# Performance work log

Measured on AMD Instinct MI355X. Metric: run time of the kernel, lower is better.

The kernel has to match this reference:

```python
import jax, jax.numpy as jnp
import numpy as np

EMBED_DIM = 512
NUM_HEADS = 8
GLOBAL_MIX = 0.5


def setup_inputs() -> dict:
    key = jax.random.key(0)
    ks = jax.random.split(key, 7)
    B, L, E = 8, 1024, EMBED_DIM
    s = 1.0 / np.sqrt(E)
    x = jax.random.normal(ks[0], (B, L, E), dtype=jnp.float32)
    mask = jax.random.randint(ks[1], (B, L), 0, 2) > 0  # True = valid token
    Wq = jax.random.normal(ks[2], (E, E), dtype=jnp.float32) * s
    Wk = jax.random.normal(ks[3], (E, E), dtype=jnp.float32) * s
    Wv = jax.random.normal(ks[4], (E, E), dtype=jnp.float32) * s
    Wo = jax.random.normal(ks[5], (E, E), dtype=jnp.float32) * s
    G = jax.random.normal(ks[6], (L, L), dtype=jnp.float32)
    return {"x": x, "mask": mask, "Wq": Wq, "Wk": Wk, "Wv": Wv, "Wo": Wo, "G": G}


def _tanh_mha(x, mask, Wq, Wk, Wv, Wo, G):
    B, L, E = x.shape
    H = NUM_HEADS
    D = E // H
    scale = 1.0 / np.sqrt(D)
    dt = x.dtype
    fmax = jnp.finfo(dt).max
    tiny = jnp.finfo(dt).tiny

    def split_heads(t):  # (B,L,E) -> (B,H,L,D)
        return t.reshape(B, L, H, D).transpose(0, 2, 1, 3)

    q = split_heads(x @ Wq.T)
    k = split_heads(x @ Wk.T)
    v = split_heads(x @ Wv.T)

    scores = jnp.tanh(jnp.einsum('bhqd,bhkd->bhqk', q, k) * scale)
    key_valid = mask[:, None, None, :]  # (B,1,1,L)
    scores = jnp.where(key_valid, scores, -jnp.inf)

    finite = jnp.isfinite(scores)
    finite_scores = jnp.where(finite, scores, -fmax)
    m = jnp.max(finite_scores, axis=(1, 2, 3), keepdims=True)  # per-sample amax over heads+q+k
    m = jnp.where(jnp.isfinite(m), m, jnp.zeros_like(m))
    exp_scores = jnp.where(finite, jnp.exp(scores - m), jnp.zeros_like(scores))

    mf = mask.astype(dt)
    exp_scores = exp_scores * mf[:, None, None, :] * mf[:, None, :, None]
    denom = jnp.maximum(exp_scores.sum(axis=(1, 2, 3), keepdims=True), tiny)
    weights = exp_scores / denom
    # dropout p=0 -> identity; renorm pass kept for faithfulness
    renorm = jnp.maximum(weights.sum(axis=(1, 2, 3), keepdims=True), tiny)
    weights = weights / renorm

    # learnable global attention: softmax rows, clamp, mask, normalize over (q,k)
    activated = jnp.maximum(jax.nn.softmax(G, axis=-1), 0.0)  # (L,L)
    gscores = activated[None] * mf[:, None, :] * mf[:, :, None]  # (B,L,L)
    gsums = jnp.maximum(gscores.sum(axis=(1, 2), keepdims=True), tiny)
    gnorm = (gscores / gsums)[:, None]  # (B,1,L,L)
    weights = (1.0 - GLOBAL_MIX) * weights + GLOBAL_MIX * gnorm

    attended = jnp.einsum('bhqk,bhkd->bhqd', weights, v)
    attended = attended * mf[:, None, :, None]
    attended = attended.transpose(0, 2, 1, 3).reshape(B, L, E)
    return attended @ Wo.T


def reference(x, mask, Wq, Wk, Wv, Wo, G):
    return _tanh_mha(x, mask, Wq, Wk, Wv, Wo, G)
```

## Files before the change

kernel.cpp:

```cpp
#include <hip/hip_runtime.h>
#include <math.h>

#define B_ 8
#define L_ 1024
#define E_ 512
#define H_ 8
#define D_ 64
#define QSZ (B_*H_*L_*D_)
#define BLE ((size_t)B_*L_*E_)
#define TINYF 1.175494350822287508e-38f
#define SWK(r) ((((r) ^ ((r) >> 3))) & 7)

typedef unsigned short u16;
typedef __attribute__((ext_vector_type(8))) short bfrag;
typedef __attribute__((ext_vector_type(4))) float ffrag;
typedef __attribute__((ext_vector_type(16))) float ffrag16;
typedef __attribute__((ext_vector_type(4))) short vshort4;

#if __has_builtin(__builtin_amdgcn_exp2f)
#define EXP2F(x) __builtin_amdgcn_exp2f(x)
#else
#define EXP2F(x) __expf((x) * 0.6931471805599453f)
#endif
#if __has_builtin(__builtin_amdgcn_rcpf)
#define RCPF(x) __builtin_amdgcn_rcpf(x)
#else
#define RCPF(x) (1.0f / (x))
#endif

__device__ __forceinline__ u16 f2b(float f) {
  unsigned u = __float_as_uint(f);
  u += 0x7fffu + ((u >> 16) & 1u);
  return (u16)(u >> 16);
}
__device__ __forceinline__ unsigned pk2(float a, float b) {
  unsigned ua = __float_as_uint(a); ua += 0x7fffu + ((ua >> 16) & 1u);
  unsigned ub = __float_as_uint(b); ub += 0x7fffu + ((ub >> 16) & 1u);
  return (ua >> 16) | (ub & 0xffff0000u);
}
__device__ __forceinline__ float blo(unsigned u) { return __uint_as_float(u << 16); }
__device__ __forceinline__ float bhi(unsigned u) { return __uint_as_float(u & 0xffff0000u); }

__device__ __forceinline__ bfrag cvt8v(const float* __restrict__ src) {
  float4 a = *(const float4*)src;
  float4 b = *(const float4*)(src + 4);
  bfrag r;
  r[0]=(short)f2b(a.x); r[1]=(short)f2b(a.y); r[2]=(short)f2b(a.z); r[3]=(short)f2b(a.w);
  r[4]=(short)f2b(b.x); r[5]=(short)f2b(b.y); r[6]=(short)f2b(b.z); r[7]=(short)f2b(b.w);
  return r;
}

__device__ __forceinline__ void gll16(const void* g, void* l) {
  __builtin_amdgcn_global_load_lds(
      (const __attribute__((address_space(1))) void*)g,
      (__attribute__((address_space(3))) void*)l, 16, 0, 0);
}

__global__ __launch_bounds__(256) void prep_softmax_k(
    const float* __restrict__ x, const float* __restrict__ Wq,
    const float* __restrict__ Wk, const float* __restrict__ Wv,
    const float* __restrict__ Wo, const float* __restrict__ G,
    const int* __restrict__ mask,
    u16* __restrict__ xb, u16* __restrict__ Wb, u16* __restrict__ actb,
    float* __restrict__ R) {
  const int bid = blockIdx.x, t = threadIdx.x;
  __shared__ float sred[8];
  __shared__ float rred[4][8];
  if (bid < 2048) {
    size_t c = (size_t)bid * 256 + t;
    *(bfrag*)&xb[c * 8] = cvt8v(x + c * 8);
    return;
  }
  if (bid < 2560) {
    const int c2 = bid - 2048;
    const float* src = (c2 < 128) ? Wq : (c2 < 256) ? Wk : (c2 < 384) ? Wv : Wo;
    const size_t base = (size_t)(c2 >> 7) * 262144;
    const size_t cc = (size_t)(c2 & 127) * 256 + t;
    *(bfrag*)&Wb[base + cc * 8] = cvt8v(src + cc * 8);
    return;
  }
  const int q = bid - 2560;
  const int w = t >> 6, lane = t & 63;
  float4 g4 = ((const float4*)(G + (size_t)q * 1024))[t];
  float m = fmaxf(fmaxf(g4.x, g4.y), fmaxf(g4.z, g4.w));
#pragma unroll
  for (int off = 32; off > 0; off >>= 1) m = fmaxf(m, __shfl_down(m, off));
  if (lane == 0) sred[w] = m;
  __syncthreads();
  m = fmaxf(fmaxf(sred[0], sred[1]), fmaxf(sred[2], sred[3]));
  float e0 = __expf(g4.x - m), e1 = __expf(g4.y - m);
  float e2 = __expf(g4.z - m), e3 = __expf(g4.w - m);
  float s = e0 + e1 + e2 + e3;
#pragma unroll
  for (int off = 32; off > 0; off >>= 1) s += __shfl_down(s, off);
  if (lane == 0) sred[4 + w] = s;
  __syncthreads();
  const float inv = 1.0f / (sred[4] + sred[5] + sred[6] + sred[7]);
  const unsigned p0 = pk2(e0 * inv, e1 * inv);
  const unsigned p1 = pk2(e2 * inv, e3 * inv);
  *(uint2*)&actb[(size_t)q * 1024 + t * 4] = make_uint2(p0, p1);
  const float r0 = blo(p0), r1 = bhi(p0);
  const float r2 = blo(p1), r3 = bhi(p1);
  float rd[8];
#pragma unroll
  for (int b = 0; b < 8; ++b) {
    const int* mkp = mask + b * 1024 + t * 4;
    rd[b] = (mkp[0] ? r0 : 0.f) + (mkp[1] ? r1 : 0.f) +
            (mkp[2] ? r2 : 0.f) + (mkp[3] ? r3 : 0.f);
#pragma unroll
    for (int off = 32; off > 0; off >>= 1) rd[b] += __shfl_down(rd[b], off);
  }
  if (lane == 0)
#pragma unroll
    for (int b = 0; b < 8; ++b) rred[w][b] = rd[b];
  __syncthreads();
  if (t < 8) R[q * 8 + t] = rred[0][t] + rred[1][t] + rred[2][t] + rred[3][t];
}

__global__ __launch_bounds__(256) void proj_k(
    const u16* __restrict__ xb, const u16* __restrict__ Wb,
    const int* __restrict__ mask, const float* __restrict__ R,
    float* __restrict__ sums,
    u16* __restrict__ Qb, u16* __restrict__ Kb, u16* __restrict__ Vtb) {
  const int m0 = blockIdx.x * 128;
  const int n0 = blockIdx.y * 128;
  __shared__ __align__(16) u16 As[128 * 64];
  __shared__ __align__(16) u16 Bs[128 * 64];
  __shared__ float rr[4][8];
  const int t = threadIdx.x, w = t >> 6, lane = t & 63;
  const int l15 = lane & 15, quad = lane >> 4;
  const int mq = (w >> 1) * 64, nq = (w & 1) * 64;

  if (blockIdx.x == 0 && blockIdx.y == 0) {
    float a8[8] = {0,0,0,0,0,0,0,0};
    for (int q = t; q < 1024; q += 256)
#pragma unroll
      for (int b = 0; b < 8; ++b)
        if (mask[b * 1024 + q]) a8[b] += R[q * 8 + b];
#pragma unroll
    for (int b = 0; b < 8; ++b) {
#pragma unroll
      for (int off = 32; off > 0; off >>= 1) a8[b] += __shfl_down(a8[b], off);
    }
    if (lane == 0)
#pragma unroll
      for (int b = 0; b < 8; ++b) rr[w][b] = a8[b];
    __syncthreads();
    if (t < 8) {
      sums[t] = 0.0f;
      sums[8 + t] = rr[0][t] + rr[1][t] + rr[2][t] + rr[3][t];
    }
  }

  const ffrag fz = {0.f, 0.f, 0.f, 0.f};
  ffrag acc[4][4];
#pragma unroll
  for (int i = 0; i < 4; ++i)
#pragma unroll
    for (int j = 0; j < 4; ++j) acc[i][j] = fz;

  for (int kk = 0; kk < 512; kk += 64) {
    __syncthreads();
#pragma unroll
    for (int j = 0; j < 4; ++j) {
      const int c = w * 256 + j * 64 + lane;
      const int row = c >> 3, ck = (c & 7) ^ (row & 7);
      gll16(xb + (size_t)(m0 + row) * 512 + kk + ck * 8,
            &As[(size_t)(w * 256 + j * 64) * 8]);
    }
#pragma unroll
    for (int j = 0; j < 4; ++j) {
      const int c = w * 256 + j * 64 + lane;
      const int row = c >> 3, ck = (c & 7) ^ (row & 7);
      gll16(Wb + (size_t)(n0 + row) * 512 + kk + ck * 8,
            &Bs[(size_t)(w * 256 + j * 64) * 8]);
    }
    __syncthreads();
#pragma unroll
    for (int s = 0; s < 2; ++s) {
      bfrag av[4], bv[4];
#pragma unroll
      for (int i = 0; i < 4; ++i) {
        const int ar = mq + i * 16 + l15;
        av[i] = *(const bfrag*)&As[ar * 64 + (((quad + 4 * s) ^ (ar & 7)) << 3)];
        const int br = nq + i * 16 + l15;
        bv[i] = *(const bfrag*)&Bs[br * 64 + (((quad + 4 * s) ^ (br & 7)) << 3)];
      }
#pragma unroll
      for (int i = 0; i < 4; ++i)
#pragma unroll
        for (int j = 0; j < 4; ++j)
          acc[i][j] = __builtin_amdgcn_mfma_f32_16x16x32_bf16(av[i], bv[j], acc[i][j], 0, 0, 0);
    }
  }
  const int z = n0 >> 9;
  const int c0 = n0 & 511;
#pragma unroll
  for (int i = 0; i < 4; ++i) {
    const int mbase = m0 + mq + i * 16 + quad * 4;
    const int b = mbase >> 10, l0 = mbase & 1023;
#pragma unroll
    for (int j = 0; j < 4; ++j) {
      const int nc = c0 + nq + j * 16 + l15;
      const int h = nc >> 6, d = nc & 63;
      if (z == 0) {
        u16* dst = Qb + ((size_t)(b * 8 + h) * 1024 + l0) * 64 + d;
#pragma unroll
        for (int r = 0; r < 4; ++r) dst[(size_t)r * 64] = f2b(acc[i][j][r]);
      } else if (z == 1) {
        u16* dst = Kb + ((size_t)(b * 8 + h) * 1024 + l0) * 64 + d;
#pragma unroll
        for (int r = 0; r < 4; ++r) dst[(size_t)r * 64] = f2b(acc[i][j][r]);
      } else {
        vshort4 vs;
#pragma unroll
        for (int r = 0; r < 4; ++r)
          vs[r] = (short)(mask[b * 1024 + l0 + r] ? f2b(acc[i][j][r]) : (u16)0);
        *(vshort4*)(Vtb + ((size_t)(b * 8 + h) * 64 + d) * 1024 + l0) = vs;
      }
    }
  }
}

__global__ __launch_bounds__(256) void attn_k(
    const u16* __restrict__ Qb, const u16* __restrict__ Kb,
    const u16* __restrict__ Vtb, const u16* __restrict__ actb,
    const int* __restrict__ mask,
    u16* __restrict__ AEb, u16* __restrict__ AGb, float* __restrict__ denom) {
  const int qt = blockIdx.x;
  const int bh = blockIdx.y;
  const int b = bh >> 3, h = bh & 7;
  __shared__ __align__(16) u16 Ks[64 * 64];
  __shared__ __align__(16) u16 Vs[64 * 64];
  __shared__ __align__(16) u16 Acts[64 * 64];
  __shared__ __align__(16) u16 Es[64 * 64];
  __shared__ __align__(16) u16 Ms[1024];
  __shared__ float red4[4];
  const int t = threadIdx.x, w = t >> 6, lane = t & 63;
  const int l31 = lane & 31, hi = lane >> 5;
  const int qsb = w >> 1, msb = w & 1;
  const int qpb = w & 1, dpb = w >> 1;

  const u16* Kg = Kb + (size_t)bh * 65536;
  const u16* Vg = Vtb + (size_t)bh * 65536;
  const u16* Ag = actb + (size_t)(qt * 64) * 1024;

  const u16* Qrow = Qb + ((size_t)bh * 1024 + qt * 64 + qsb * 32 + l31) * 64;
  bfrag qf[4];
#pragma unroll
  for (int ko = 0; ko < 4; ++ko) qf[ko] = *(const bfrag*)(Qrow + ko * 16 + hi * 8);

  {
    int4 mi = *(const int4*)(mask + b * 1024 + t * 4);
    vshort4 mv;
    mv[0] = mi.x ? (short)0x3F80 : (short)0; mv[1] = mi.y ? (short)0x3F80 : (short)0;
    mv[2] = mi.z ? (short)0x3F80 : (short)0; mv[3] = mi.w ? (short)0x3F80 : (short)0;
    *(vshort4*)&Ms[t * 4] = mv;
  }

  auto stageK = [&](int kt) {
#pragma unroll
    for (int j = 0; j < 2; ++j) {
      const int c = w * 128 + j * 64 + lane;
      const int row = c >> 3, ck = (c & 7) ^ SWK(row);
      gll16(Kg + (size_t)(kt * 64 + row) * 64 + ck * 8,
            &Ks[(size_t)(w * 128 + j * 64) * 8]);
    }
  };
  auto stageV = [&](int kt) {
#pragma unroll
    for (int j = 0; j < 2; ++j) {
      const int c = w * 128 + j * 64 + lane;
      const int row = c >> 3, ck = (c & 7) ^ SWK(row);
      gll16(Vg + (size_t)row * 1024 + kt * 64 + ck * 8,
            &Vs[(size_t)(w * 128 + j * 64) * 8]);
    }
  };
  auto stageA = [&](int kt) {
#pragma unroll
    for (int j = 0; j < 2; ++j) {
      const int c = w * 128 + j * 64 + lane;
      const int row = c >> 3, ck = (c & 7) ^ SWK(row);
      gll16(Ag + (size_t)row * 1024 + kt * 64 + ck * 8,
            &Acts[(size_t)(w * 128 + j * 64) * 8]);
    }
  };

  stageK(0); stageV(0); stageA(0);
  __syncthreads();

  ffrag16 accE, accG, dacc;
#pragma unroll
  for (int i = 0; i < 16; ++i) { accE[i] = 0.f; accG[i] = 0.f; dacc[i] = 0.f; }

  for (int kt = 0; kt < 16; ++kt) {
    ffrag16 st;
#pragma unroll
    for (int i = 0; i < 16; ++i) st[i] = 0.f;
    const int krow = msb * 32 + l31;
    const int kk7 = SWK(krow);
#pragma unroll
    for (int ko = 0; ko < 4; ++ko) {
      bfrag ak = *(const bfrag*)&Ks[krow * 64 + (((ko * 2 + hi) ^ kk7) << 3)];
      st = __builtin_amdgcn_mfma_f32_32x32x16_bf16(ak, qf[ko], st, 0, 0, 0);
    }
    const int qrow = qsb * 32 + l31;
    const int qk7 = SWK(qrow);
#pragma unroll
    for (int g = 0; g < 4; ++g) {
      float ee[4];
#pragma unroll
      for (int r = 0; r < 4; ++r) {
        const float tt = EXP2F(st[4 * g + r] * 0.360673760222f);
        ee[r] = EXP2F(RCPF(tt + 1.0f) * -2.88539008178f);
      }
      const int k0 = msb * 32 + g * 8 + hi * 4;
      *(uint2*)&Es[qrow * 64 + (((k0 >> 3) ^ qk7) << 3) + (k0 & 7)] =
          make_uint2(pk2(ee[0], ee[1]), pk2(ee[2], ee[3]));
    }
    __syncthreads();
    if (kt < 15) stageK(kt + 1);

    const int erow = qpb * 32 + l31;
    const int ek7 = SWK(erow);
    const int vrow = dpb * 32 + l31;
    const int vk7 = SWK(vrow);
#pragma unroll
    for (int ko = 0; ko < 4; ++ko) {
      const int co = ko * 2 + hi;
      bfrag ea = *(const bfrag*)&Es[erow * 64 + ((co ^ ek7) << 3)];
      bfrag aa = *(const bfrag*)&Acts[erow * 64 + ((co ^ ek7) << 3)];
      bfrag bv = *(const bfrag*)&Vs[vrow * 64 + ((co ^ vk7) << 3)];
      accE = __builtin_amdgcn_mfma_f32_32x32x16_bf16(ea, bv, accE, 0, 0, 0);
      accG = __builtin_amdgcn_mfma_f32_32x32x16_bf16(aa, bv, accG, 0, 0, 0);
      if (dpb == 0) {
        bfrag bm = *(const bfrag*)&Ms[kt * 64 + ko * 16 + hi * 8];
        dacc = __builtin_amdgcn_mfma_f32_32x32x16_bf16(ea, bm, dacc, 0, 0, 0);
      }
    }
    __syncthreads();
    if (kt < 15) { stageV(kt + 1); stageA(kt + 1); }
  }

  const size_t obase = ((size_t)(b * 1024 + qt * 64 + qpb * 32)) * 512
                       + h * 64 + dpb * 32 + l31;
#pragma unroll
  for (int r = 0; r < 16; ++r) {
    const int qloc = (r & 3) + 8 * (r >> 2) + 4 * hi;
    AEb[obase + (size_t)qloc * 512] = f2b(accE[r]);
    AGb[obase + (size_t)qloc * 512] = f2b(accG[r]);
  }
  float dsumv = 0.0f;
  if (l31 == 0 && dpb == 0) {
    const int qb0 = b * 1024 + qt * 64 + qpb * 32 + 4 * hi;
#pragma unroll
    for (int r = 0; r < 16; ++r) {
      const int q = qb0 + (r & 3) + 8 * (r >> 2);
      dsumv += mask[q] ? dacc[r] : 0.0f;
    }
    red4[qpb * 2 + hi] = dsumv;
  }
  __syncthreads();
  if (t == 0) atomicAdd(denom + b, red4[0] + red4[1] + red4[2] + red4[3]);
}

__global__ __launch_bounds__(256) void o_proj_k(
    const u16* __restrict__ AEb, const u16* __restrict__ AGb,
    const int* __restrict__ mask, const float* __restrict__ sums,
    const u16* __restrict__ Wb, float* __restrict__ out) {
  const int m0 = blockIdx.x * 128;
  const int n0 = blockIdx.y * 128;
  const int b = m0 >> 10;
  const float c1 = 0.5f / fmaxf(sums[b], TINYF);
  const float c2 = 0.5f / fmaxf(sums[8 + b], TINYF);
  __shared__ __align__(16) u16 As[128 * 64];
  __shared__ __align__(16) u16 Bs[128 * 64];
  const int t = threadIdx.x, w = t >> 6, lane = t & 63;
  const int l15 = lane & 15, quad = lane >> 4;
  const int mq = (w >> 1) * 64, nq = (w & 1) * 64;
  int rowi[4]; float c1r[4], c2r[4];
#pragma unroll
  for (int i = 0; i < 4; ++i) {
    const int c = t + i * 256;
    rowi[i] = c >> 3;
    const int mqv = mask[b * 1024 + ((m0 + rowi[i]) & 1023)];
    c1r[i] = mqv ? c1 : 0.0f;
    c2r[i] = mqv ? c2 : 0.0f;
  }
  const ffrag fz = {0.f, 0.f, 0.f, 0.f};
  ffrag acc[4][4];
#pragma unroll
  for (int i = 0; i < 4; ++i)
#pragma unroll
    for (int j = 0; j < 4; ++j) acc[i][j] = fz;

  for (int kk = 0; kk < 512; kk += 64) {
    __syncthreads();
#pragma unroll
    for (int i = 0; i < 4; ++i) {
      const int c = t + i * 256;
      const int row = rowi[i], ck = c & 7;
      const size_t gofs = (size_t)(m0 + row) * 512 + kk + ck * 8;
      uint4 ua = *(const uint4*)(AEb + gofs);
      uint4 ug = *(const uint4*)(AGb + gofs);
      const float a1 = c1r[i], a2 = c2r[i];
      uint4 res;
      res.x = pk2(a1 * blo(ua.x) + a2 * blo(ug.x), a1 * bhi(ua.x) + a2 * bhi(ug.x));
      res.y = pk2(a1 * blo(ua.y) + a2 * blo(ug.y), a1 * bhi(ua.y) + a2 * bhi(ug.y));
      res.z = pk2(a1 * blo(ua.z) + a2 * blo(ug.z), a1 * bhi(ua.z) + a2 * bhi(ug.z));
      res.w = pk2(a1 * blo(ua.w) + a2 * blo(ug.w), a1 * bhi(ua.w) + a2 * bhi(ug.w));
      *(uint4*)&As[row * 64 + ((ck ^ (row & 7)) << 3)] = res;
    }
#pragma unroll
    for (int j = 0; j < 4; ++j) {
      const int c = w * 256 + j * 64 + lane;
      const int row = c >> 3, ck = (c & 7) ^ (row & 7);
      gll16(Wb + (size_t)(1536 + n0 + row) * 512 + kk + ck * 8,
            &Bs[(size_t)(w * 256 + j * 64) * 8]);
    }
    __syncthreads();
#pragma unroll
    for (int s = 0; s < 2; ++s) {
      bfrag av[4], bv[4];
#pragma unroll
      for (int i = 0; i < 4; ++i) {
        const int ar = mq + i * 16 + l15;
        av[i] = *(const bfrag*)&As[ar * 64 + (((quad + 4 * s) ^ (ar & 7)) << 3)];
        const int br = nq + i * 16 + l15;
        bv[i] = *(const bfrag*)&Bs[br * 64 + (((quad + 4 * s) ^ (br & 7)) << 3)];
      }
#pragma unroll
      for (int i = 0; i < 4; ++i)
#pragma unroll
        for (int j = 0; j < 4; ++j)
          acc[i][j] = __builtin_amdgcn_mfma_f32_16x16x32_bf16(av[i], bv[j], acc[i][j], 0, 0, 0);
    }
  }
#pragma unroll
  for (int i = 0; i < 4; ++i) {
    const int mbase = m0 + mq + i * 16 + quad * 4;
#pragma unroll
    for (int j = 0; j < 4; ++j) {
      const int n = n0 + nq + j * 16 + l15;
#pragma unroll
      for (int r = 0; r < 4; ++r)
        out[(size_t)(mbase + r) * 512 + n] = acc[i][j][r];
    }
  }
}

extern "C" void kernel_launch(void* const* d_in, const int* in_sizes, int n_in,
                              void* d_out, int out_size, void* d_ws, size_t ws_size,
                              hipStream_t stream) {
  const float* x  = (const float*)d_in[0];
  const int* mask = (const int*)d_in[1];
  const float* Wq = (const float*)d_in[2];
  const float* Wk = (const float*)d_in[3];
  const float* Wv = (const float*)d_in[4];
  const float* Wo = (const float*)d_in[5];
  const float* G  = (const float*)d_in[6];
  float* out = (float*)d_out;

  u16* xb   = (u16*)d_ws;
  u16* Wb   = xb + (size_t)8192 * 512;
  u16* Qb   = Wb + (size_t)2048 * 512;
  u16* Kb   = Qb + QSZ;
  u16* Vtb  = Kb + QSZ;
  u16* actb = Vtb + QSZ;
  u16* AEb  = actb + (size_t)1024 * 1024;
  u16* AGb  = AEb + BLE;
  float* R  = (float*)(AGb + BLE);
  float* SUMS = R + 8192;

  prep_softmax_k<<<3584, 256, 0, stream>>>(x, Wq, Wk, Wv, Wo, G, mask, xb, Wb, actb, R);
  proj_k<<<dim3(64, 12), 256, 0, stream>>>(xb, Wb, mask, R, SUMS, Qb, Kb, Vtb);
  attn_k<<<dim3(16, 64), 256, 0, stream>>>(Qb, Kb, Vtb, actb, mask, AEb, AGb, SUMS);
  o_proj_k<<<dim3(64, 4), 256, 0, stream>>>(AEb, AGb, mask, SUMS, Wb, out);
}
```

Before: 189.2 us.

## Split global-attention product into dedicated GEMM blocks fused into attention launch

The global mix term act·V is identical across heads, so it is computed as a per-batch GEMM (1024x1024 by 1024x512) in 512 extra blocks instead of being recomputed inside each head's attention tile. The attention blocks drop the Acts staging and the accG MFMA, which cuts their shared memory and register pressure, and they share one kernel launch with the GEMM blocks. The GEMM blocks reread V transposed across all heads, and the two block types have different workloads, which may cause load imbalance.

```diff
diff --git a/kernel.cpp b/kernel.cpp
--- a/kernel.cpp
+++ b/kernel.cpp
@@ -222,28 +222,96 @@
   }
 }
 
-__global__ __launch_bounds__(256) void attn_k(
+__global__ __launch_bounds__(256) void attn_gv_k(
     const u16* __restrict__ Qb, const u16* __restrict__ Kb,
     const u16* __restrict__ Vtb, const u16* __restrict__ actb,
     const int* __restrict__ mask,
     u16* __restrict__ AEb, u16* __restrict__ AGb, float* __restrict__ denom) {
-  const int qt = blockIdx.x;
-  const int bh = blockIdx.y;
+  __shared__ __align__(16) u16 POOL[13320];
+  const int t = threadIdx.x, w = t >> 6, lane = t & 63;
+  const int l15 = lane & 15, quad = lane >> 4;
+
+  if (blockIdx.x < 512) {
+    u16* As = POOL;
+    u16* Bs = POOL + 4096;
+    const int mt = blockIdx.x & 127, nt = blockIdx.x >> 7;
+    const int m0 = mt * 64, n0 = nt * 128;
+    const int b = mt >> 4;
+    const int q0 = (mt & 15) * 64;
+    const int mq = (w >> 1) * 32, nq = (w & 1) * 64;
+    const ffrag fz = {0.f, 0.f, 0.f, 0.f};
+    ffrag acc[2][4];
+#pragma unroll
+    for (int i = 0; i < 2; ++i)
+#pragma unroll
+      for (int j = 0; j < 4; ++j) acc[i][j] = fz;
+
+    for (int kk = 0; kk < 1024; kk += 64) {
+      __syncthreads();
+#pragma unroll
+      for (int j = 0; j < 2; ++j) {
+        const int c = w * 128 + j * 64 + lane;
+        const int row = c >> 3, ck = (c & 7) ^ (row & 7);
+        gll16(actb + (size_t)(q0 + row) * 1024 + kk + ck * 8,
+              &As[(size_t)(w * 128 + j * 64) * 8]);
+      }
+#pragma unroll
+      for (int j = 0; j < 4; ++j) {
+        const int c = w * 256 + j * 64 + lane;
+        const int row = c >> 3, ck = (c & 7) ^ (row & 7);
+        gll16(Vtb + (size_t)(b * 512 + n0 + row) * 1024 + kk + ck * 8,
+              &Bs[(size_t)(w * 256 + j * 64) * 8]);
+      }
+      __syncthreads();
+#pragma unroll
+      for (int s = 0; s < 2; ++s) {
+        bfrag av[2], bv[4];
+#pragma unroll
+        for (int i = 0; i < 2; ++i) {
+          const int ar = mq + i * 16 + l15;
+          av[i] = *(const bfrag*)&As[ar * 64 + (((quad + 4 * s) ^ (ar & 7)) << 3)];
+        }
+#pragma unroll
+        for (int j = 0; j < 4; ++j) {
+          const int br = nq + j * 16 + l15;
+          bv[j] = *(const bfrag*)&Bs[br * 64 + (((quad + 4 * s) ^ (br & 7)) << 3)];
+        }
+#pragma unroll
+        for (int i = 0; i < 2; ++i)
+#pragma unroll
+          for (int j = 0; j < 4; ++j)
+            acc[i][j] = __builtin_amdgcn_mfma_f32_16x16x32_bf16(av[i], bv[j], acc[i][j], 0, 0, 0);
+      }
+    }
+#pragma unroll
+    for (int i = 0; i < 2; ++i) {
+      const int mbase = m0 + mq + i * 16 + quad * 4;
+#pragma unroll
+      for (int j = 0; j < 4; ++j) {
+        const int n = n0 + nq + j * 16 + l15;
+#pragma unroll
+        for (int r = 0; r < 4; ++r)
+          AGb[(size_t)(mbase + r) * 512 + n] = f2b(acc[i][j][r]);
+      }
+    }
+    return;
+  }
+
+  const int aid = blockIdx.x - 512;
+  const int qt = aid & 15;
+  const int bh = aid >> 4;
   const int b = bh >> 3, h = bh & 7;
-  __shared__ __align__(16) u16 Ks[64 * 64];
-  __shared__ __align__(16) u16 Vs[64 * 64];
-  __shared__ __align__(16) u16 Acts[64 * 64];
-  __shared__ __align__(16) u16 Es[64 * 64];
-  __shared__ __align__(16) u16 Ms[1024];
-  __shared__ float red4[4];
-  const int t = threadIdx.x, w = t >> 6, lane = t & 63;
+  u16* Ks = POOL;
+  u16* Vs = POOL + 4096;
+  u16* Es = POOL + 8192;
+  u16* Ms = POOL + 12288;
+  float* red4 = (float*)(POOL + 13312);
   const int l31 = lane & 31, hi = lane >> 5;
   const int qsb = w >> 1, msb = w & 1;
   const int qpb = w & 1, dpb = w >> 1;
 
   const u16* Kg = Kb + (size_t)bh * 65536;
   const u16* Vg = Vtb + (size_t)bh * 65536;
-  const u16* Ag = actb + (size_t)(qt * 64) * 1024;
 
   const u16* Qrow = Qb + ((size_t)bh * 1024 + qt * 64 + qsb * 32 + l31) * 64;
   bfrag qf[4];
@@ -276,22 +344,13 @@
             &Vs[(size_t)(w * 128 + j * 64) * 8]);
     }
   };
-  auto stageA = [&](int kt) {
-#pragma unroll
-    for (int j = 0; j < 2; ++j) {
-      const int c = w * 128 + j * 64 + lane;
-      const int row = c >> 3, ck = (c & 7) ^ SWK(row);
-      gll16(Ag + (size_t)row * 1024 + kt * 64 + ck * 8,
-            &Acts[(size_t)(w * 128 + j * 64) * 8]);
-    }
-  };
-
-  stageK(0); stageV(0); stageA(0);
+
+  stageK(0); stageV(0);
   __syncthreads();
 
-  ffrag16 accE, accG, dacc;
-#pragma unroll
-  for (int i = 0; i < 16; ++i) { accE[i] = 0.f; accG[i] = 0.f; dacc[i] = 0.f; }
+  ffrag16 accE, dacc;
+#pragma unroll
+  for (int i = 0; i < 16; ++i) { accE[i] = 0.f; dacc[i] = 0.f; }
 
   for (int kt = 0; kt < 16; ++kt) {
     ffrag16 st;
@@ -329,17 +388,15 @@
     for (int ko = 0; ko < 4; ++ko) {
       const int co = ko * 2 + hi;
       bfrag ea = *(const bfrag*)&Es[erow * 64 + ((co ^ ek7) << 3)];
-      bfrag aa = *(const bfrag*)&Acts[erow * 64 + ((co ^ ek7) << 3)];
       bfrag bv = *(const bfrag*)&Vs[vrow * 64 + ((co ^ vk7) << 3)];
       accE = __builtin_amdgcn_mfma_f32_32x32x16_bf16(ea, bv, accE, 0, 0, 0);
-      accG = __builtin_amdgcn_mfma_f32_32x32x16_bf16(aa, bv, accG, 0, 0, 0);
       if (dpb == 0) {
         bfrag bm = *(const bfrag*)&Ms[kt * 64 + ko * 16 + hi * 8];
         dacc = __builtin_amdgcn_mfma_f32_32x32x16_bf16(ea, bm, dacc, 0, 0, 0);
       }
     }
     __syncthreads();
-    if (kt < 15) { stageV(kt + 1); stageA(kt + 1); }
+    if (kt < 15) stageV(kt + 1);
   }
 
   const size_t obase = ((size_t)(b * 1024 + qt * 64 + qpb * 32)) * 512
@@ -348,7 +405,6 @@
   for (int r = 0; r < 16; ++r) {
     const int qloc = (r & 3) + 8 * (r >> 2) + 4 * hi;
     AEb[obase + (size_t)qloc * 512] = f2b(accE[r]);
-    AGb[obase + (size_t)qloc * 512] = f2b(accG[r]);
   }
   float dsumv = 0.0f;
   if (l31 == 0 && dpb == 0) {
@@ -474,6 +530,6 @@
 
   prep_softmax_k<<<3584, 256, 0, stream>>>(x, Wq, Wk, Wv, Wo, G, mask, xb, Wb, actb, R);
   proj_k<<<dim3(64, 12), 256, 0, stream>>>(xb, Wb, mask, R, SUMS, Qb, Kb, Vtb);
-  attn_k<<<dim3(16, 64), 256, 0, stream>>>(Qb, Kb, Vtb, actb, mask, AEb, AGb, SUMS);
+  attn_gv_k<<<1536, 256, 0, stream>>>(Qb, Kb, Vtb, actb, mask, AEb, AGb, SUMS);
   o_proj_k<<<dim3(64, 4), 256, 0, stream>>>(AEb, AGb, mask, SUMS, Wb, out);
 }
```

Result: faster. 183.8 us (-2.8%).
